# Kernel optimization log

Hardware: AMD Instinct MI355X
Metric: run time of the kernel (lower is better)

The kernel has to match this reference:

```python
import jax, jax.numpy as jnp
import numpy as np

B, S, H = 8, 4096, 2048
HINT, WS, STRIDE = 4, 16, 8
MLP_H = 64


def _window_starts():
    # Mirrors the torch loop: break when the window is shorter than window_size//2.
    starts = []
    for s in range(0, S, STRIDE):
        e = min(s + WS, S)
        if e - s < WS // 2:
            break
        starts.append(s)
    return np.asarray(starts, dtype=np.int32)  # [W] = [512]


def setup_inputs() -> dict:
    key = jax.random.key(0)
    k1, k2, k3, k4, k5 = jax.random.split(key, 5)
    return {
        "hidden_states": jax.random.normal(k1, (B, S, H), jnp.float32),
        "attention_mask": jax.random.randint(k2, (B, S), 0, 2).astype(jnp.int32),
        "hint_features": jax.random.normal(k3, (B, S, HINT), jnp.float32),
        "W1": jax.random.normal(k4, (H + HINT, MLP_H), jnp.float32) * 0.02,
        "b1": jnp.zeros((MLP_H,), jnp.float32),
        "W2": jax.random.normal(k5, (MLP_H, 1), jnp.float32) * 0.02,
        "b2": jnp.zeros((1,), jnp.float32),
    }


def reference(hidden_states, attention_mask, hint_features, W1, b1, W2, b2):
    starts = jnp.asarray(_window_starts())               # [W]
    idx = starts[:, None] + jnp.arange(WS)               # [W, ws]
    pos_valid = (idx < S).astype(jnp.float32)            # [W, ws]  (pads past seq end)
    idxc = jnp.minimum(idx, S - 1)

    # [B, W, ws] combined attention + in-bounds mask
    mask = attention_mask[:, idxc].astype(jnp.float32) * pos_valid[None]
    denom = jnp.clip(jnp.sum(mask, axis=-1, keepdims=True), 1.0, None)  # [B, W, 1]

    # Gather overlapping windows once, pool with a single einsum each.
    win_h = hidden_states[:, idxc]                        # [B, W, ws, H]
    win_f = hint_features[:, idxc]                        # [B, W, ws, HINT]
    pooled_h = jnp.einsum('bwk,bwkh->bwh', mask, win_h) / denom
    pooled_f = jnp.einsum('bwk,bwkh->bwh', mask, win_f) / denom
    pooled = jnp.concatenate([pooled_h, pooled_f], axis=-1)  # [B, W, H+HINT]

    # MLP (dropout is identity at inference); torch GELU default = exact erf.
    h = jax.nn.gelu(pooled @ W1 + b1, approximate=False)
    window_logits = (h @ W2 + b2)[..., 0]                 # [B, W]
    window_mask = (jnp.sum(mask, axis=-1) > 0).astype(jnp.float32)  # [B, W]
    return window_logits, window_mask
```

## Files before the change

kernel.cpp:

```cpp
#include <hip/hip_runtime.h>
#include <math.h>

#define B_      8
#define S_      4096
#define H_      2048
#define HINT_   4
#define WS_     16
#define STRIDE_ 8
#define MLPH_   64
#define NW_     512
#define WPB_    8
#define ROWS_   72
#define KT_     68
#define KPAD_   2176
#define LDK_    2184
#define NT_     4
#define PLD_    66

typedef float  floatx4 __attribute__((ext_vector_type(4)));
typedef short  shortx8 __attribute__((ext_vector_type(8)));

__device__ __forceinline__ unsigned short f2b(float x) {
    unsigned u = __float_as_uint(x);
    u += 0x7FFFu + ((u >> 16) & 1u);
    return (unsigned short)(u >> 16);
}

__global__ void prep_w1(const float* __restrict__ W1, unsigned short* __restrict__ W1B) {
    const int blk  = blockIdx.x;
    const int nt   = blk / KT_;
    const int kt   = blk % KT_;
    const int lane = threadIdx.x;
    const int n     = nt * 16 + (lane & 15);
    const int kbase = kt * 32 + (lane >> 4) * 8;
    unsigned short tmp[8];
#pragma unroll
    for (int j = 0; j < 8; ++j) {
        const int k = kbase + j;
        const float v = (k < (H_ + HINT_)) ? W1[(size_t)k * MLPH_ + n] : 0.0f;
        tmp[j] = f2b(v);
    }
    *(uint4*)(W1B + (((size_t)nt * KT_ + kt) * 64 + lane) * 8) = *(const uint4*)tmp;
}

__global__ __launch_bounds__(512, 8) void wbh_kernel(
    const float* __restrict__ hidden,
    const int*   __restrict__ amask,
    const float* __restrict__ hintf,
    const float* __restrict__ b1,
    const float* __restrict__ W2,
    const float* __restrict__ b2,
    const unsigned short* __restrict__ W1B,
    float* __restrict__ out)
{
    __shared__ unsigned short pooledLds[WPB_ * LDK_];
    __shared__ float amLds[ROWS_];
    __shared__ float hintLds[ROWS_ * HINT_];
    __shared__ float rinvLds[WPB_];
    __shared__ unsigned amBitsLds[WPB_ + 1];
    __shared__ float partLds[WPB_ * 2 * PLD_];

    const int tid = threadIdx.x;
    const int bid = blockIdx.x;
    const int gid   = (bid & 7) * 64 + (bid >> 3);
    const int b     = gid >> 6;
    const int chunk = gid & 63;
    const int w0    = chunk * WPB_;
    const int s0    = chunk * (WPB_ * STRIDE_);

    if (tid < 8 * 62) {
        const int row = tid / 62, cc = tid % 62;
        *(unsigned*)&pooledLds[row * LDK_ + 2052 + cc * 2] = 0u;
    }
    if (tid < ROWS_) {
        const int p = s0 + tid;
        amLds[tid] = (p < S_) ? (float)amask[b * S_ + p] : 0.0f;
    }
    if (tid < ROWS_ * HINT_) {
        const int rr = tid >> 2;
        const int p  = s0 + rr;
        hintLds[tid] = (p < S_) ? hintf[((size_t)b * S_ + p) * HINT_ + (tid & 3)] : 0.0f;
    }
    __syncthreads();

    if (tid < WPB_) {
        float s = 0.f;
#pragma unroll
        for (int k = 0; k < WS_; ++k) s += amLds[tid * STRIDE_ + k];
        rinvLds[tid] = 1.0f / fmaxf(s, 1.0f);
        out[(size_t)(B_ * NW_) + (size_t)b * NW_ + w0 + tid] = (s > 0.f) ? 1.0f : 0.0f;
    }
    if (tid < WPB_ + 1) {
        unsigned bits = 0;
#pragma unroll
        for (int k = 0; k < STRIDE_; ++k)
            bits |= (amLds[tid * STRIDE_ + k] != 0.0f ? 1u : 0u) << k;
        amBitsLds[tid] = bits;
    }
    __syncthreads();

    const int c0 = tid * 4;
    const float* rowBase = hidden + ((size_t)b * S_ + s0) * H_ + c0;

    floatx4 prev = (floatx4){0.f, 0.f, 0.f, 0.f};
#pragma unroll
    for (int g = 0; g <= WPB_; ++g) {
        const unsigned bits =
            (unsigned)__builtin_amdgcn_readfirstlane((int)amBitsLds[g]);
        floatx4 cur = (floatx4){0.f, 0.f, 0.f, 0.f};
#pragma unroll
        for (int k = 0; k < STRIDE_; ++k) {
            if (bits & (1u << k)) {
                cur += *(const floatx4*)(rowBase + (size_t)(g * STRIDE_ + k) * H_);
            }
        }
        if (g >= 1) {
            const int w = g - 1;
            const floatx4 s = prev + cur;
            const float r = rinvLds[w];
            unsigned short q[4];
            q[0] = f2b(s.x * r); q[1] = f2b(s.y * r);
            q[2] = f2b(s.z * r); q[3] = f2b(s.w * r);
            *(uint2*)(&pooledLds[w * LDK_ + c0]) = *(const uint2*)q;
        }
        prev = cur;
    }

    if (tid < WPB_ * HINT_) {
        const int w = tid >> 2, hc = tid & 3;
        float s = 0.f;
#pragma unroll
        for (int k = 0; k < WS_; ++k) {
            const int rr = w * STRIDE_ + k;
            s += amLds[rr] * hintLds[rr * HINT_ + hc];
        }
        pooledLds[w * LDK_ + H_ + hc] = f2b(s * rinvLds[w]);
    }
    __syncthreads();

    const int wid  = tid >> 6;
    const int lane = tid & 63;
    const int nt   = wid & 3;
    const int kh   = wid >> 2;
    {
        floatx4 dacc = (floatx4){0.f, 0.f, 0.f, 0.f};
        const unsigned short* aBase =
            pooledLds + (lane & 7) * LDK_ + (lane >> 4) * 8 + kh * 34 * 32;
        const unsigned short* bBase =
            W1B + (((size_t)nt * KT_ + kh * 34) * 64 + lane) * 8;
#pragma unroll 4
        for (int kt = 0; kt < 34; ++kt) {
            const shortx8 af = *(const shortx8*)(aBase + kt * 32);
            const shortx8 bf = *(const shortx8*)(bBase + (size_t)kt * 64 * 8);
            dacc = __builtin_amdgcn_mfma_f32_16x16x32_bf16(af, bf, dacc, 0, 0, 0);
        }
        if (lane < 32) {
            const int m0 = (lane >> 4) * 4;
            const int j  = nt * 16 + (lane & 15);
#pragma unroll
            for (int r = 0; r < 4; ++r)
                partLds[((m0 + r) * 2 + kh) * PLD_ + j] = dacc[r];
        }
    }
    __syncthreads();

    {
        const int m = tid >> 6;
        const int j = tid & 63;
        const float a = partLds[(m * 2) * PLD_ + j] + partLds[(m * 2 + 1) * PLD_ + j]
                      + b1[j];
        float g = 0.5f * a * (1.0f + erff(a * 0.70710678118654752f)) * W2[j];
#pragma unroll
        for (int off = 32; off > 0; off >>= 1) g += __shfl_down(g, off, 64);
        if (j == 0) out[(size_t)b * NW_ + w0 + m] = g + b2[0];
    }
}

extern "C" void kernel_launch(void* const* d_in, const int* in_sizes, int n_in,
                              void* d_out, int out_size, void* d_ws, size_t ws_size,
                              hipStream_t stream) {
    const float* hidden = (const float*)d_in[0];
    const int*   amask  = (const int*)d_in[1];
    const float* hintf  = (const float*)d_in[2];
    const float* W1     = (const float*)d_in[3];
    const float* b1     = (const float*)d_in[4];
    const float* W2     = (const float*)d_in[5];
    const float* b2     = (const float*)d_in[6];
    float* out          = (float*)d_out;

    unsigned short* W1B = (unsigned short*)d_ws;

    prep_w1<<<NT_ * KT_, 64, 0, stream>>>(W1, W1B);
    wbh_kernel<<<B_ * (NW_ / WPB_), 512, 0, stream>>>(
        hidden, amask, hintf, b1, W2, b2, W1B, out);
}
```

Baseline: 349.2 us.

## Issue all masked row loads up front and drop K-split in MLP GEMM

The pooling loop now loads all eight rows of each stride group at once, redirecting masked rows to a dummy address, and uses FMA with the mask. This replaces the branchy per-bit conditional loads and raises memory-level parallelism. Hint features are read straight from global memory with a mask check instead of being staged in LDS. The MFMA stage now uses 4 waves over the full K range, removing the K-split partial reduction. Launch bounds drop from 8 to 6, leaving more registers per thread. The costs are half the waves idling in the GEMM, a longer serial MFMA chain, and redundant loads of the dummy row.

```diff
diff --git a/kernel.cpp b/kernel.cpp
--- a/kernel.cpp
+++ b/kernel.cpp
@@ -43,7 +43,7 @@
     *(uint4*)(W1B + (((size_t)nt * KT_ + kt) * 64 + lane) * 8) = *(const uint4*)tmp;
 }
 
-__global__ __launch_bounds__(512, 8) void wbh_kernel(
+__global__ __launch_bounds__(512, 6) void wbh_kernel(
     const float* __restrict__ hidden,
     const int*   __restrict__ amask,
     const float* __restrict__ hintf,
@@ -55,10 +55,8 @@
 {
     __shared__ unsigned short pooledLds[WPB_ * LDK_];
     __shared__ float amLds[ROWS_];
-    __shared__ float hintLds[ROWS_ * HINT_];
     __shared__ float rinvLds[WPB_];
-    __shared__ unsigned amBitsLds[WPB_ + 1];
-    __shared__ float partLds[WPB_ * 2 * PLD_];
+    __shared__ float partLds[WPB_ * PLD_];
 
     const int tid = threadIdx.x;
     const int bid = blockIdx.x;
@@ -76,11 +74,6 @@
         const int p = s0 + tid;
         amLds[tid] = (p < S_) ? (float)amask[b * S_ + p] : 0.0f;
     }
-    if (tid < ROWS_ * HINT_) {
-        const int rr = tid >> 2;
-        const int p  = s0 + rr;
-        hintLds[tid] = (p < S_) ? hintf[((size_t)b * S_ + p) * HINT_ + (tid & 3)] : 0.0f;
-    }
     __syncthreads();
 
     if (tid < WPB_) {
@@ -90,13 +83,6 @@
         rinvLds[tid] = 1.0f / fmaxf(s, 1.0f);
         out[(size_t)(B_ * NW_) + (size_t)b * NW_ + w0 + tid] = (s > 0.f) ? 1.0f : 0.0f;
     }
-    if (tid < WPB_ + 1) {
-        unsigned bits = 0;
-#pragma unroll
-        for (int k = 0; k < STRIDE_; ++k)
-            bits |= (amLds[tid * STRIDE_ + k] != 0.0f ? 1u : 0u) << k;
-        amBitsLds[tid] = bits;
-    }
     __syncthreads();
 
     const int c0 = tid * 4;
@@ -105,14 +91,25 @@
     floatx4 prev = (floatx4){0.f, 0.f, 0.f, 0.f};
 #pragma unroll
     for (int g = 0; g <= WPB_; ++g) {
-        const unsigned bits =
-            (unsigned)__builtin_amdgcn_readfirstlane((int)amBitsLds[g]);
+        float am[STRIDE_];
+        const float* ptr[STRIDE_];
+#pragma unroll
+        for (int k = 0; k < STRIDE_; ++k) {
+            const int rr = g * STRIDE_ + k;
+            am[k]  = amLds[rr];
+            ptr[k] = (am[k] != 0.0f) ? (rowBase + (size_t)rr * H_) : rowBase;
+        }
+        floatx4 v[STRIDE_];
+#pragma unroll
+        for (int k = 0; k < STRIDE_; ++k) v[k] = *(const floatx4*)ptr[k];
+
         floatx4 cur = (floatx4){0.f, 0.f, 0.f, 0.f};
 #pragma unroll
         for (int k = 0; k < STRIDE_; ++k) {
-            if (bits & (1u << k)) {
-                cur += *(const floatx4*)(rowBase + (size_t)(g * STRIDE_ + k) * H_);
-            }
+            cur.x = fmaf(am[k], v[k].x, cur.x);
+            cur.y = fmaf(am[k], v[k].y, cur.y);
+            cur.z = fmaf(am[k], v[k].z, cur.z);
+            cur.w = fmaf(am[k], v[k].w, cur.w);
         }
         if (g >= 1) {
             const int w = g - 1;
@@ -132,7 +129,11 @@
 #pragma unroll
         for (int k = 0; k < WS_; ++k) {
             const int rr = w * STRIDE_ + k;
-            s += amLds[rr] * hintLds[rr * HINT_ + hc];
+            const float amv = amLds[rr];
+            float hv = 0.f;
+            if (amv != 0.0f)
+                hv = hintf[((size_t)b * S_ + (s0 + rr)) * HINT_ + hc];
+            s += amv * hv;
         }
         pooledLds[w * LDK_ + H_ + hc] = f2b(s * rinvLds[w]);
     }
@@ -140,26 +141,22 @@
 
     const int wid  = tid >> 6;
     const int lane = tid & 63;
-    const int nt   = wid & 3;
-    const int kh   = wid >> 2;
-    {
+    if (wid < NT_) {
         floatx4 dacc = (floatx4){0.f, 0.f, 0.f, 0.f};
-        const unsigned short* aBase =
-            pooledLds + (lane & 7) * LDK_ + (lane >> 4) * 8 + kh * 34 * 32;
-        const unsigned short* bBase =
-            W1B + (((size_t)nt * KT_ + kh * 34) * 64 + lane) * 8;
+        const unsigned short* aBase = pooledLds + (lane & 7) * LDK_ + (lane >> 4) * 8;
+        const unsigned short* bBase = W1B + ((size_t)wid * KT_ * 64 + lane) * 8;
 #pragma unroll 4
-        for (int kt = 0; kt < 34; ++kt) {
+        for (int kt = 0; kt < KT_; ++kt) {
             const shortx8 af = *(const shortx8*)(aBase + kt * 32);
             const shortx8 bf = *(const shortx8*)(bBase + (size_t)kt * 64 * 8);
             dacc = __builtin_amdgcn_mfma_f32_16x16x32_bf16(af, bf, dacc, 0, 0, 0);
         }
         if (lane < 32) {
             const int m0 = (lane >> 4) * 4;
-            const int j  = nt * 16 + (lane & 15);
+            const int j  = wid * 16 + (lane & 15);
 #pragma unroll
             for (int r = 0; r < 4; ++r)
-                partLds[((m0 + r) * 2 + kh) * PLD_ + j] = dacc[r];
+                partLds[(m0 + r) * PLD_ + j] = dacc[r];
         }
     }
     __syncthreads();
@@ -167,8 +164,7 @@
     {
         const int m = tid >> 6;
         const int j = tid & 63;
-        const float a = partLds[(m * 2) * PLD_ + j] + partLds[(m * 2 + 1) * PLD_ + j]
-                      + b1[j];
+        const float a = partLds[m * PLD_ + j] + b1[j];
         float g = 0.5f * a * (1.0f + erff(a * 0.70710678118654752f)) * W2[j];
 #pragma unroll
         for (int off = 32; off > 0; off >>= 1) g += __shfl_down(g, off, 64);
```

Result: no change. 349.2 us (-0.0%).
